# Kernel optimization log

Measured on AMD Instinct MI355X. Metric: run time of the kernel, lower is better.

The kernel has to match this reference:

```python
import jax, jax.numpy as jnp
import numpy as np

DROPOUT_P = 0.5

def _gcn_conv(h, W, b, src, dst, norm, self_norm, n):
    # h: [N, Din] -> [N, Dout]; symmetric-normalized aggregation with self loops
    h = h @ W
    msg = h[src] * norm[:, None]                       # [E, Dout]
    agg = jax.ops.segment_sum(msg, dst, num_segments=n)
    return agg + h * self_norm[:, None] + b


def setup_inputs() -> dict:
    key = jax.random.key(0)
    ks = jax.random.split(key, 8)
    N, E, D_IN, D_OUT = 50000, 800000, 512, 256
    H = 2 * D_OUT  # 512
    x = jax.random.normal(ks[0], (N, D_IN), dtype=jnp.float32)
    edge_index = jax.random.randint(ks[1], (2, E), 0, N, dtype=jnp.int64)
    s = 1.0 / np.sqrt(D_IN)
    W1 = jax.random.uniform(ks[2], (D_IN, H), jnp.float32, -s, s)
    b1 = jnp.zeros((H,), jnp.float32)
    s2 = 1.0 / np.sqrt(H)
    Wmu = jax.random.uniform(ks[3], (H, D_OUT), jnp.float32, -s2, s2)
    bmu = jnp.zeros((D_OUT,), jnp.float32)
    Wls = jax.random.uniform(ks[4], (H, D_OUT), jnp.float32, -s2, s2)
    bls = jnp.zeros((D_OUT,), jnp.float32)
    return {"x": x, "edge_index": edge_index, "W1": W1, "b1": b1,
            "Wmu": Wmu, "bmu": bmu, "Wls": Wls, "bls": bls}


def reference(x, edge_index, W1, b1, Wmu, bmu, Wls, bls):
    n = x.shape[0]
    src, dst = edge_index[0], edge_index[1]
    # GCN symmetric normalization with self loops: deg includes +1 self loop
    deg = jax.ops.segment_sum(jnp.ones_like(dst, dtype=x.dtype), dst, num_segments=n) + 1.0
    dinv = jax.lax.rsqrt(deg)
    norm = dinv[src] * dinv[dst]     # per-edge norm
    self_norm = dinv * dinv          # self-loop norm = 1/deg
    # dropout (train mode, deterministic mask)
    keep = jax.random.bernoulli(jax.random.key(42), 1.0 - DROPOUT_P, x.shape)
    h = jnp.where(keep, x / (1.0 - DROPOUT_P), 0.0)
    h = jax.nn.relu(_gcn_conv(h, W1, b1, src, dst, norm, self_norm, n))
    mu = _gcn_conv(h, Wmu, bmu, src, dst, norm, self_norm, n)
    logstd = _gcn_conv(h, Wls, bls, src, dst, norm, self_norm, n)
    return (mu, logstd)
```

## Files before the change

### kernel.cpp

```cpp
#include <hip/hip_runtime.h>
#include <hip/hip_bf16.h>

typedef __hip_bfloat16 bf16;
typedef __attribute__((ext_vector_type(8))) short short8;
typedef __attribute__((ext_vector_type(4))) float f32x4;

__device__ __forceinline__ float bfu(unsigned short b) {
    unsigned u = ((unsigned)b) << 16;
    float f;
    __builtin_memcpy(&f, &u, 4);
    return f;
}
__device__ __forceinline__ unsigned short f2b(float f) {
    return (unsigned short)(__hip_bfloat16_raw(__float2bfloat16(f)).x);
}

__device__ __forceinline__ void gl_lds16(const void* g, void* l) {
    __builtin_amdgcn_global_load_lds(
        (const __attribute__((address_space(1))) void*)g,
        (__attribute__((address_space(3))) void*)l, 16, 0, 0);
}

__device__ __forceinline__ bool keep_elem(unsigned idx) {
    const unsigned k0 = 0u, k1 = 42u;
    const unsigned k2 = k0 ^ k1 ^ 0x1BD11BDAu;
    unsigned x0 = k0;
    unsigned x1 = idx + k1;
#define TF_QR(R) { x0 += x1; x1 = (x1 << R) | (x1 >> (32 - R)); x1 ^= x0; }
    TF_QR(13) TF_QR(15) TF_QR(26) TF_QR(6)
    x0 += k1; x1 += k2 + 1u;
    TF_QR(17) TF_QR(29) TF_QR(16) TF_QR(24)
    x0 += k2; x1 += k0 + 2u;
    TF_QR(13) TF_QR(15) TF_QR(26) TF_QR(6)
    x0 += k0; x1 += k1 + 3u;
    TF_QR(17) TF_QR(29) TF_QR(16) TF_QR(24)
    x0 += k1; x1 += k2 + 4u;
    TF_QR(13) TF_QR(15) TF_QR(26) TF_QR(6)
    x0 += k2; x1 += k0 + 5u;
#undef TF_QR
    return (((x0 ^ x1) >> 31) & 1u) == 0u;
}

__global__ void detect_edges_k(const unsigned* __restrict__ w, int* __restrict__ flag) {
    __shared__ unsigned red[256];
    unsigned v = 0;
    for (int i = threadIdx.x; i < 2048; i += 256) v |= w[2 * i + 1];
    red[threadIdx.x] = v;
    __syncthreads();
    for (int s = 128; s > 0; s >>= 1) {
        if (threadIdx.x < s) red[threadIdx.x] |= red[threadIdx.x + s];
        __syncthreads();
    }
    if (threadIdx.x == 0) flag[0] = (red[0] == 0u) ? 1 : 0;
}

__global__ void detect_f32_k(const unsigned short* __restrict__ w,
                             int* __restrict__ flag, int fidx) {
    __shared__ int red[256];
    int cnt = 0;
    for (int i = threadIdx.x; i < 1024; i += 256) {
        unsigned short b = w[2 * i];
        int e = (b >> 7) & 0xFF;
        if ((b & 0x7FFF) == 0 || (e >= 100 && e < 140)) cnt++;
    }
    red[threadIdx.x] = cnt;
    __syncthreads();
    for (int s = 128; s > 0; s >>= 1) {
        if (threadIdx.x < s) red[threadIdx.x] += red[threadIdx.x + s];
        __syncthreads();
    }
    if (threadIdx.x == 0) flag[fidx] = (red[0] < 614) ? 1 : 0;
}

__global__ void convert_edges_k(const void* __restrict__ src, int* __restrict__ out,
                                int twoE, const int* __restrict__ flag) {
    int i = blockIdx.x * 256 + threadIdx.x;
    if (i >= twoE) return;
    if (flag[0]) out[i] = (int)((const unsigned long long*)src)[i];
    else         out[i] = ((const int*)src)[i];
}

__global__ void canon_x_drop_k(const void* __restrict__ src, bf16* __restrict__ dst,
                               int n8, const int* __restrict__ flag) {
    int i = blockIdx.x * 256 + threadIdx.x;
    if (i >= n8) return;
    float v[8];
    if (flag[1]) {
        const f32x4* p = (const f32x4*)src;
        f32x4 a = p[2 * i], b = p[2 * i + 1];
#pragma unroll
        for (int k = 0; k < 4; ++k) { v[k] = a[k]; v[4 + k] = b[k]; }
    } else {
        short8 u = ((const short8*)src)[i];
#pragma unroll
        for (int k = 0; k < 8; ++k) v[k] = bfu((unsigned short)u[k]);
    }
    unsigned base = (unsigned)i * 8u;
    short8 o;
#pragma unroll
    for (int k = 0; k < 8; ++k) {
        float f = keep_elem(base + k) ? v[k] * 2.0f : 0.0f;
        o[k] = (short)f2b(f);
    }
    ((short8*)dst)[i] = o;
}

__global__ void canon_k(const void* __restrict__ src, bf16* __restrict__ dst,
                        int n, const int* __restrict__ flag, int fidx) {
    int i = blockIdx.x * 256 + threadIdx.x;
    if (i >= n) return;
    if (flag[fidx]) dst[i] = __float2bfloat16(((const float*)src)[i]);
    else            dst[i] = ((const bf16*)src)[i];
}

__global__ void canon_transpose_k(const void* __restrict__ src, unsigned short* __restrict__ dst,
                                  int K, int Nn, const int* __restrict__ flag, int fidx) {
    __shared__ unsigned short tile[16][17];
    int k0 = blockIdx.x * 16, n0 = blockIdx.y * 16;
    int k = k0 + threadIdx.y, n = n0 + threadIdx.x;
    unsigned short v;
    if (flag[fidx]) v = f2b(((const float*)src)[(size_t)k * Nn + n]);
    else            v = ((const unsigned short*)src)[(size_t)k * Nn + n];
    tile[threadIdx.y][threadIdx.x] = v;
    __syncthreads();
    int nn = n0 + threadIdx.y, kk = k0 + threadIdx.x;
    dst[(size_t)nn * K + kk] = tile[threadIdx.x][threadIdx.y];
}

__global__ void zero_int_k(int* __restrict__ p, int n) {
    int i = blockIdx.x * 256 + threadIdx.x;
    if (i < n) p[i] = 0;
}
__global__ void deg_count_k(const int* __restrict__ edges, int* __restrict__ degi,
                            int E, int n) {
    int e = blockIdx.x * 256 + threadIdx.x;
    if (e >= E) return;
    int d = edges[E + e];
    d = (d < 0) ? 0 : (d >= n ? n - 1 : d);
    atomicAdd(&degi[d], 1);
}
__global__ void dinv_k(const int* __restrict__ degi, float* __restrict__ dinv, int n) {
    int i = blockIdx.x * 256 + threadIdx.x;
    if (i < n) dinv[i] = rsqrtf(1.0f + (float)degi[i]);
}
__global__ void block_sums_k(const int* __restrict__ deg, int* __restrict__ partial, int n) {
    __shared__ int sh[256];
    int i = blockIdx.x * 256 + threadIdx.x;
    sh[threadIdx.x] = (i < n) ? deg[i] : 0;
    __syncthreads();
    for (int s = 128; s > 0; s >>= 1) {
        if (threadIdx.x < s) sh[threadIdx.x] += sh[threadIdx.x + s];
        __syncthreads();
    }
    if (threadIdx.x == 0) partial[blockIdx.x] = sh[0];
}
__global__ void scan_partials_k(int* __restrict__ partial, int G) {
    __shared__ int sh[256];
    int v = (threadIdx.x < G) ? partial[threadIdx.x] : 0;
    sh[threadIdx.x] = v;
    __syncthreads();
    for (int s = 1; s < 256; s <<= 1) {
        int t = 0;
        if (threadIdx.x >= s) t = sh[threadIdx.x - s];
        __syncthreads();
        sh[threadIdx.x] += t;
        __syncthreads();
    }
    if (threadIdx.x < G) partial[threadIdx.x] = sh[threadIdx.x] - v;
}
__global__ void scan_block_k(const int* __restrict__ deg, const int* __restrict__ partial,
                             int* __restrict__ row_ptr, int n) {
    __shared__ int sh[256];
    int i = blockIdx.x * 256 + threadIdx.x;
    int v = (i < n) ? deg[i] : 0;
    sh[threadIdx.x] = v;
    __syncthreads();
    for (int s = 1; s < 256; s <<= 1) {
        int t = 0;
        if (threadIdx.x >= s) t = sh[threadIdx.x - s];
        __syncthreads();
        sh[threadIdx.x] += t;
        __syncthreads();
    }
    int incl = sh[threadIdx.x];
    int base = partial[blockIdx.x];
    if (i < n) row_ptr[i] = base + incl - v;
    if (i == n - 1) row_ptr[n] = base + incl;
}
__global__ void fill_k(const int* __restrict__ edges, const int* __restrict__ row_ptr,
                       int* __restrict__ cnt, int* __restrict__ col, int E, int n) {
    int e = blockIdx.x * 256 + threadIdx.x;
    if (e >= E) return;
    int s = edges[e], d = edges[E + e];
    s = (s < 0) ? 0 : (s >= n ? n - 1 : s);
    d = (d < 0) ? 0 : (d >= n ? n - 1 : d);
    int pos = row_ptr[d] + atomicAdd(&cnt[d], 1);
    col[pos] = s;
}

__global__ __launch_bounds__(256) void gemm_mfma_k(
    const bf16* __restrict__ A, const bf16* __restrict__ Bt,
    bf16* __restrict__ Cb, float* __restrict__ Cf, const bf16* __restrict__ bias,
    int M, int Nn, int K) {
    __shared__ short sA[128 * 32];
    __shared__ short sB[128 * 32];
    const int tid = threadIdx.x;
    const int lane = tid & 63;
    const int w = tid >> 6;
    const int m0 = blockIdx.x * 128;
    const int n0 = blockIdx.y * 128;
    const int wm = (w >> 1) * 64;
    const int wn = (w & 1) * 64;

    f32x4 acc[4][4] = {};

    const int srow = lane >> 2;
    const int scol = (lane & 3) * 8;

    for (int kk = 0; kk < K; kk += 32) {
#pragma unroll
        for (int q = 0; q < 2; ++q) {
            int r = q * 64 + w * 16 + srow;
            int grow = m0 + r; if (grow >= M) grow = M - 1;
            gl_lds16(A + (size_t)grow * K + kk + scol, &sA[q * 2048 + w * 512 + lane * 8]);
        }
#pragma unroll
        for (int q = 0; q < 2; ++q) {
            int r = q * 64 + w * 16 + srow;
            gl_lds16(Bt + (size_t)(n0 + r) * K + kk + scol, &sB[q * 2048 + w * 512 + lane * 8]);
        }
        __syncthreads();

        const int fr = lane & 15;
        const int fk = (lane >> 4) * 8;
        short8 af[4], bfr[4];
#pragma unroll
        for (int i = 0; i < 4; ++i)
            af[i] = *(const short8*)&sA[(wm + i * 16 + fr) * 32 + fk];
#pragma unroll
        for (int j = 0; j < 4; ++j)
            bfr[j] = *(const short8*)&sB[(wn + j * 16 + fr) * 32 + fk];
#pragma unroll
        for (int i = 0; i < 4; ++i)
#pragma unroll
            for (int j = 0; j < 4; ++j)
                acc[i][j] = __builtin_amdgcn_mfma_f32_16x16x32_bf16(
                    af[i], bfr[j], acc[i][j], 0, 0, 0);
        __syncthreads();
    }

    const int crow = (lane >> 4) * 4;
    const int ccol = lane & 15;
#pragma unroll
    for (int i = 0; i < 4; ++i) {
#pragma unroll
        for (int r = 0; r < 4; ++r) {
            int row = m0 + wm + i * 16 + crow + r;
            if (row >= M) continue;
            if (Cf) {
                float* cp = Cf + (size_t)row * Nn + n0 + wn;
#pragma unroll
                for (int j = 0; j < 4; ++j) {
                    int c = j * 16 + ccol;
                    cp[c] = acc[i][j][r] + __bfloat162float(bias[n0 + wn + c]);
                }
            } else {
                bf16* cp = Cb + (size_t)row * Nn + n0 + wn;
#pragma unroll
                for (int j = 0; j < 4; ++j)
                    cp[j * 16 + ccol] = __float2bfloat16(acc[i][j][r]);
            }
        }
    }
}

__global__ __launch_bounds__(256) void gather_k(
    const bf16* __restrict__ t, const int* __restrict__ row_ptr,
    const int* __restrict__ col, const float* __restrict__ dinv,
    const bf16* __restrict__ bias, bf16* __restrict__ outp, int mode, int N) {
    const int node = blockIdx.x * 4 + (threadIdx.x >> 6);
    if (node >= N) return;
    const int lane = threadIdx.x & 63;
    const short8* tp = (const short8*)t;
    const int beg = row_ptr[node];
    const int end = row_ptr[node + 1];
    const float dv = dinv[node];
    float acc[8] = {0.f, 0.f, 0.f, 0.f, 0.f, 0.f, 0.f, 0.f};

    int e = beg;
    for (; e + 4 <= end; e += 4) {
        int s0 = col[e + 0], s1 = col[e + 1], s2 = col[e + 2], s3 = col[e + 3];
        float w0 = dinv[s0] * dv, w1 = dinv[s1] * dv;
        float w2 = dinv[s2] * dv, w3 = dinv[s3] * dv;
        short8 u0 = tp[(size_t)s0 * 64 + lane];
        short8 u1 = tp[(size_t)s1 * 64 + lane];
        short8 u2 = tp[(size_t)s2 * 64 + lane];
        short8 u3 = tp[(size_t)s3 * 64 + lane];
#pragma unroll
        for (int k = 0; k < 8; ++k) {
            acc[k] += w0 * bfu((unsigned short)u0[k]);
            acc[k] += w1 * bfu((unsigned short)u1[k]);
            acc[k] += w2 * bfu((unsigned short)u2[k]);
            acc[k] += w3 * bfu((unsigned short)u3[k]);
        }
    }
    for (; e < end; ++e) {
        int s = col[e];
        float w = dinv[s] * dv;
        short8 u = tp[(size_t)s * 64 + lane];
#pragma unroll
        for (int k = 0; k < 8; ++k) acc[k] += w * bfu((unsigned short)u[k]);
    }
    {
        short8 u = tp[(size_t)node * 64 + lane];
        float w = dv * dv;
#pragma unroll
        for (int k = 0; k < 8; ++k) acc[k] += w * bfu((unsigned short)u[k]);
    }
    if (mode == 1) {
        short8 bs = ((const short8*)bias)[lane];
#pragma unroll
        for (int k = 0; k < 8; ++k) {
            acc[k] += bfu((unsigned short)bs[k]);
            acc[k] = fmaxf(acc[k], 0.f);
        }
    }
    short8 o;
#pragma unroll
    for (int k = 0; k < 8; ++k) o[k] = (short)f2b(acc[k]);
    ((short8*)outp)[(size_t)node * 64 + lane] = o;
}

extern "C" void kernel_launch(void* const* d_in, const int* in_sizes, int n_in,
                              void* d_out, int out_size, void* d_ws, size_t ws_size,
                              hipStream_t stream) {
    const void* xin   = d_in[0];
    const void* ei    = d_in[1];
    const void* W1in  = d_in[2];
    const void* b1in  = d_in[3];
    const void* Wmuin = d_in[4];
    const void* bmuin = d_in[5];
    const void* Wlsin = d_in[6];
    const void* blsin = d_in[7];
    float* out = (float*)d_out;

    const int H    = in_sizes[3];
    const int DOUT = in_sizes[5];
    const int DIN  = in_sizes[2] / H;
    const int N    = in_sizes[0] / DIN;
    const int E    = in_sizes[1] / 2;
    const int G    = (N + 255) / 256;

    char* ws = (char*)d_ws;
    size_t off = 0;
    auto alloc = [&](size_t bytes) {
        void* p = ws + off;
        off = (off + bytes + 255) & ~(size_t)255;
        return p;
    };
    int*   flag    = (int*)alloc(256);
    int*   edges   = (int*)alloc((size_t)2 * E * 4);
    int*   degi    = (int*)alloc((size_t)N * 4);
    int*   row_ptr = (int*)alloc((size_t)(N + 1) * 4);
    int*   cnt     = (int*)alloc((size_t)N * 4);
    int*   partial = (int*)alloc((size_t)G * 4);
    int*   col     = (int*)alloc((size_t)E * 4);
    float* dinv    = (float*)alloc((size_t)N * 4);
    bf16*  t1      = (bf16*)alloc((size_t)N * H * 2);
    bf16*  g1      = (bf16*)alloc((size_t)N * H * 2);
    bf16*  xdrop   = (bf16*)alloc((size_t)N * DIN * 2);
    bf16*  W1t     = (bf16*)alloc((size_t)DIN * H * 2);
    bf16*  Wmut    = (bf16*)alloc((size_t)H * DOUT * 2);
    bf16*  Wlst    = (bf16*)alloc((size_t)H * DOUT * 2);
    bf16*  b1c     = (bf16*)alloc((size_t)H * 2);
    bf16*  bmuc    = (bf16*)alloc((size_t)DOUT * 2);
    bf16*  blsc    = (bf16*)alloc((size_t)DOUT * 2);
    if (off > ws_size) return;

    const int twoE = 2 * E;
    hipLaunchKernelGGL(detect_edges_k, dim3(1), dim3(256), 0, stream, (const unsigned*)ei, flag);
    hipLaunchKernelGGL(detect_f32_k, dim3(1), dim3(256), 0, stream, (const unsigned short*)xin, flag, 1);
    hipLaunchKernelGGL(detect_f32_k, dim3(1), dim3(256), 0, stream, (const unsigned short*)W1in, flag, 2);

    hipLaunchKernelGGL(convert_edges_k, dim3((twoE + 255) / 256), dim3(256), 0, stream,
                       ei, edges, twoE, flag);
    int n8 = (N * DIN) / 8;
    hipLaunchKernelGGL(canon_x_drop_k, dim3((n8 + 255) / 256), dim3(256), 0, stream,
                       xin, xdrop, n8, flag);
    hipLaunchKernelGGL(canon_transpose_k, dim3(DIN / 16, H / 16), dim3(16, 16), 0, stream,
                       W1in, (unsigned short*)W1t, DIN, H, flag, 2);
    hipLaunchKernelGGL(canon_transpose_k, dim3(H / 16, DOUT / 16), dim3(16, 16), 0, stream,
                       Wmuin, (unsigned short*)Wmut, H, DOUT, flag, 2);
    hipLaunchKernelGGL(canon_transpose_k, dim3(H / 16, DOUT / 16), dim3(16, 16), 0, stream,
                       Wlsin, (unsigned short*)Wlst, H, DOUT, flag, 2);
    hipLaunchKernelGGL(canon_k, dim3(2), dim3(256), 0, stream, b1in, b1c, H, flag, 2);
    hipLaunchKernelGGL(canon_k, dim3(1), dim3(256), 0, stream, bmuin, bmuc, DOUT, flag, 2);
    hipLaunchKernelGGL(canon_k, dim3(1), dim3(256), 0, stream, blsin, blsc, DOUT, flag, 2);

    hipLaunchKernelGGL(zero_int_k, dim3(G), dim3(256), 0, stream, degi, N);
    hipLaunchKernelGGL(zero_int_k, dim3(G), dim3(256), 0, stream, cnt, N);
    hipLaunchKernelGGL(deg_count_k, dim3((E + 255) / 256), dim3(256), 0, stream, edges, degi, E, N);
    hipLaunchKernelGGL(dinv_k, dim3(G), dim3(256), 0, stream, degi, dinv, N);
    hipLaunchKernelGGL(block_sums_k, dim3(G), dim3(256), 0, stream, degi, partial, N);
    hipLaunchKernelGGL(scan_partials_k, dim3(1), dim3(256), 0, stream, partial, G);
    hipLaunchKernelGGL(scan_block_k, dim3(G), dim3(256), 0, stream, degi, partial, row_ptr, N);
    hipLaunchKernelGGL(fill_k, dim3((E + 255) / 256), dim3(256), 0, stream, edges, row_ptr, cnt, col, E, N);

    hipLaunchKernelGGL(gemm_mfma_k, dim3((N + 127) / 128, H / 128), dim3(256), 0, stream,
                       xdrop, W1t, t1, (float*)nullptr, (const bf16*)nullptr, N, H, DIN);
    bf16* h1 = xdrop;
    hipLaunchKernelGGL(gather_k, dim3((N + 3) / 4), dim3(256), 0, stream,
                       t1, row_ptr, col, dinv, b1c, h1, 1, N);

    hipLaunchKernelGGL(gather_k, dim3((N + 3) / 4), dim3(256), 0, stream,
                       h1, row_ptr, col, dinv, (const bf16*)nullptr, g1, 0, N);
    hipLaunchKernelGGL(gemm_mfma_k, dim3((N + 127) / 128, DOUT / 128), dim3(256), 0, stream,
                       g1, Wmut, (bf16*)nullptr, out, bmuc, N, DOUT, H);
    hipLaunchKernelGGL(gemm_mfma_k, dim3((N + 127) / 128, DOUT / 128), dim3(256), 0, stream,
                       g1, Wlst, (bf16*)nullptr, out + (size_t)N * DOUT, blsc, N, DOUT, H);
}
```

Baseline: 679.0 us.

## Fuse mu/logstd GEMMs via concatenated weights and software-pipeline gather loop

Concatenates the transposed Wmu and Wls weights and their biases so a single GEMM over 2*DOUT output columns computes both heads. The epilogue sends each column tile to the mu or logstd output buffer. This reads the aggregated g1 matrix once instead of twice and removes one launch. The gather kernel also gets an 8-edge unrolled main loop that prefetches the next batch of column indices and degree weights while the current rows are accumulated, aiming to hide index-load latency at the cost of more registers.

```diff
diff --git a/kernel.cpp b/kernel.cpp
--- a/kernel.cpp
+++ b/kernel.cpp
@@ -200,8 +200,8 @@
 
 __global__ __launch_bounds__(256) void gemm_mfma_k(
     const bf16* __restrict__ A, const bf16* __restrict__ Bt,
-    bf16* __restrict__ Cb, float* __restrict__ Cf, const bf16* __restrict__ bias,
-    int M, int Nn, int K) {
+    bf16* __restrict__ Cb, float* __restrict__ Cf, float* __restrict__ Cf2,
+    const bf16* __restrict__ bias, int M, int Nn, int K, int split) {
     __shared__ short sA[128 * 32];
     __shared__ short sB[128 * 32];
     const int tid = threadIdx.x;
@@ -251,6 +251,13 @@
 
     const int crow = (lane >> 4) * 4;
     const int ccol = lane & 15;
+    float* fbase = Cf;
+    int nb = n0 + wn;
+    int stride = Nn;
+    if (Cf2) {
+        stride = split;
+        if (nb >= split) { fbase = Cf2; nb -= split; }
+    }
 #pragma unroll
     for (int i = 0; i < 4; ++i) {
 #pragma unroll
@@ -258,7 +265,7 @@
             int row = m0 + wm + i * 16 + crow + r;
             if (row >= M) continue;
             if (Cf) {
-                float* cp = Cf + (size_t)row * Nn + n0 + wn;
+                float* cp = fbase + (size_t)row * stride + nb;
 #pragma unroll
                 for (int j = 0; j < 4; ++j) {
                     int c = j * 16 + ccol;
@@ -288,6 +295,41 @@
     float acc[8] = {0.f, 0.f, 0.f, 0.f, 0.f, 0.f, 0.f, 0.f};
 
     int e = beg;
+    const int elim = beg + ((end - beg) & ~7);
+    if (e < elim) {
+        int c[8];
+        float w[8];
+#pragma unroll
+        for (int k = 0; k < 8; ++k) c[k] = col[e + k];
+#pragma unroll
+        for (int k = 0; k < 8; ++k) w[k] = dinv[c[k]] * dv;
+        for (;;) {
+            short8 u[8];
+#pragma unroll
+            for (int k = 0; k < 8; ++k) u[k] = tp[(size_t)c[k] * 64 + lane];
+            const int en = e + 8;
+            const bool more = en < elim;
+            int cn[8];
+            float wn2[8];
+            if (more) {
+#pragma unroll
+                for (int k = 0; k < 8; ++k) cn[k] = col[en + k];
+#pragma unroll
+                for (int k = 0; k < 8; ++k) wn2[k] = dinv[cn[k]] * dv;
+            }
+#pragma unroll
+            for (int k = 0; k < 8; ++k) {
+                const float wk = w[k];
+#pragma unroll
+                for (int j = 0; j < 8; ++j)
+                    acc[j] += wk * bfu((unsigned short)u[k][j]);
+            }
+            e = en;
+            if (!more) break;
+#pragma unroll
+            for (int k = 0; k < 8; ++k) { c[k] = cn[k]; w[k] = wn2[k]; }
+        }
+    }
     for (; e + 4 <= end; e += 4) {
         int s0 = col[e + 0], s1 = col[e + 1], s2 = col[e + 2], s3 = col[e + 3];
         float w0 = dinv[s0] * dv, w1 = dinv[s1] * dv;
@@ -370,11 +412,9 @@
     bf16*  g1      = (bf16*)alloc((size_t)N * H * 2);
     bf16*  xdrop   = (bf16*)alloc((size_t)N * DIN * 2);
     bf16*  W1t     = (bf16*)alloc((size_t)DIN * H * 2);
-    bf16*  Wmut    = (bf16*)alloc((size_t)H * DOUT * 2);
-    bf16*  Wlst    = (bf16*)alloc((size_t)H * DOUT * 2);
+    bf16*  Wcat    = (bf16*)alloc((size_t)H * 2 * DOUT * 2);
     bf16*  b1c     = (bf16*)alloc((size_t)H * 2);
-    bf16*  bmuc    = (bf16*)alloc((size_t)DOUT * 2);
-    bf16*  blsc    = (bf16*)alloc((size_t)DOUT * 2);
+    bf16*  bcat    = (bf16*)alloc((size_t)2 * DOUT * 2);
     if (off > ws_size) return;
 
     const int twoE = 2 * E;
@@ -390,12 +430,12 @@
     hipLaunchKernelGGL(canon_transpose_k, dim3(DIN / 16, H / 16), dim3(16, 16), 0, stream,
                        W1in, (unsigned short*)W1t, DIN, H, flag, 2);
     hipLaunchKernelGGL(canon_transpose_k, dim3(H / 16, DOUT / 16), dim3(16, 16), 0, stream,
-                       Wmuin, (unsigned short*)Wmut, H, DOUT, flag, 2);
+                       Wmuin, (unsigned short*)Wcat, H, DOUT, flag, 2);
     hipLaunchKernelGGL(canon_transpose_k, dim3(H / 16, DOUT / 16), dim3(16, 16), 0, stream,
-                       Wlsin, (unsigned short*)Wlst, H, DOUT, flag, 2);
+                       Wlsin, (unsigned short*)(Wcat + (size_t)DOUT * H), H, DOUT, flag, 2);
     hipLaunchKernelGGL(canon_k, dim3(2), dim3(256), 0, stream, b1in, b1c, H, flag, 2);
-    hipLaunchKernelGGL(canon_k, dim3(1), dim3(256), 0, stream, bmuin, bmuc, DOUT, flag, 2);
-    hipLaunchKernelGGL(canon_k, dim3(1), dim3(256), 0, stream, blsin, blsc, DOUT, flag, 2);
+    hipLaunchKernelGGL(canon_k, dim3(1), dim3(256), 0, stream, bmuin, bcat, DOUT, flag, 2);
+    hipLaunchKernelGGL(canon_k, dim3(1), dim3(256), 0, stream, blsin, bcat + DOUT, DOUT, flag, 2);
 
     hipLaunchKernelGGL(zero_int_k, dim3(G), dim3(256), 0, stream, degi, N);
     hipLaunchKernelGGL(zero_int_k, dim3(G), dim3(256), 0, stream, cnt, N);
@@ -407,15 +447,15 @@
     hipLaunchKernelGGL(fill_k, dim3((E + 255) / 256), dim3(256), 0, stream, edges, row_ptr, cnt, col, E, N);
 
     hipLaunchKernelGGL(gemm_mfma_k, dim3((N + 127) / 128, H / 128), dim3(256), 0, stream,
-                       xdrop, W1t, t1, (float*)nullptr, (const bf16*)nullptr, N, H, DIN);
+                       xdrop, W1t, t1, (float*)nullptr, (float*)nullptr,
+                       (const bf16*)nullptr, N, H, DIN, 0);
     bf16* h1 = xdrop;
     hipLaunchKernelGGL(gather_k, dim3((N + 3) / 4), dim3(256), 0, stream,
                        t1, row_ptr, col, dinv, b1c, h1, 1, N);
 
     hipLaunchKernelGGL(gather_k, dim3((N + 3) / 4), dim3(256), 0, stream,
                        h1, row_ptr, col, dinv, (const bf16*)nullptr, g1, 0, N);
-    hipLaunchKernelGGL(gemm_mfma_k, dim3((N + 127) / 128, DOUT / 128), dim3(256), 0, stream,
-                       g1, Wmut, (bf16*)nullptr, out, bmuc, N, DOUT, H);
-    hipLaunchKernelGGL(gemm_mfma_k, dim3((N + 127) / 128, DOUT / 128), dim3(256), 0, stream,
-                       g1, Wlst, (bf16*)nullptr, out + (size_t)N * DOUT, blsc, N, DOUT, H);
-}
+    hipLaunchKernelGGL(gemm_mfma_k, dim3((N + 127) / 128, (2 * DOUT) / 128), dim3(256), 0, stream,
+                       g1, Wcat, (bf16*)nullptr, out, out + (size_t)N * DOUT,
+                       bcat, N, 2 * DOUT, H, DOUT);
+}
```

Result: faster. 659.1 us (-2.9%).
